# Kernel tuning notes

Hardware: AMD Instinct MI355X
Metric: run time of the kernel (lower is better)

## Reference

```python
import jax, jax.numpy as jnp
import numpy as np
from jax import lax

EPS = 1e-6


def _layernorm(x, g, b, eps=1e-5):
    m = x.mean(-1, keepdims=True)
    v = x.var(-1, keepdims=True)
    return (x - m) / jnp.sqrt(v + eps) * g + b


def _causal_conv(x, w, b, dilation):
    # x: [B,S,D], w: [K, D_in, D_out] -> causal (left) padded dilated conv + GELU, residual
    k = w.shape[0]
    pad = (k - 1) * dilation
    y = lax.conv_general_dilated(
        x, w, window_strides=(1,), padding=[(pad, 0)], rhs_dilation=(dilation,),
        dimension_numbers=('NWC', 'WIO', 'NWC'))
    return x + jax.nn.gelu(y + b)


def setup_inputs() -> dict:
    key = jax.random.key(0)
    B, S, D, DC, N_LTM, K_WM, KS = 4, 2048, 1024, 256, 768, 8, 5
    ks = jax.random.split(key, 24)
    sc = 0.02

    def n(k, shape, scale=sc):
        return jax.random.normal(k, shape, jnp.float32) * scale

    return {
        'x': jax.random.normal(ks[0], (B, S, D), jnp.float32),
        'cache': jax.random.normal(ks[1], (B, N_LTM, DC), jnp.float32),
        'wm': jax.random.normal(ks[2], (B, K_WM, DC + 1), jnp.float32),
        # LTM read projections
        'Wq_ltm': n(ks[3], (D, DC)), 'Wo_ltm': n(ks[4], (DC, D)), 'wg_ltm': n(ks[5], (D,)),
        # WM read projections
        'Wq_wm': n(ks[6], (D, DC)), 'Wo_wm': n(ks[7], (DC, D)), 'wg_wm': n(ks[8], (D,)),
        # causal dilated conv stack (2 layers, k=5, dilations 1 and 2)
        'conv1_w': n(ks[9], (KS, D, D)), 'conv1_b': jnp.zeros((D,), jnp.float32),
        'conv2_w': n(ks[10], (KS, D, D)), 'conv2_b': jnp.zeros((D,), jnp.float32),
        'ln_g': jnp.ones((D,), jnp.float32), 'ln_b': jnp.zeros((D,), jnp.float32),
        # WM write (learned slot keys for addressing)
        'Wqw_wm': n(ks[11], (D, DC)), 'Ww_wm': n(ks[12], (D, DC)),
        'wm_keys': n(ks[13], (K_WM, DC), 1.0), 'wgw_wm': n(ks[14], (D,)),
        # LTM write (content-based addressing against cache)
        'Wqw_ltm': n(ks[15], (D, DC)), 'Ww_ltm': n(ks[16], (D, DC)), 'wgw_ltm': n(ks[17], (D,)),
    }


def reference(x, cache, wm, Wq_ltm, Wo_ltm, wg_ltm, Wq_wm, Wo_wm, wg_wm,
              conv1_w, conv1_b, conv2_w, conv2_b, ln_g, ln_b,
              Wqw_wm, Ww_wm, wm_keys, wgw_wm, Wqw_ltm, Ww_ltm, wgw_ltm):
    DC = cache.shape[-1]
    inv_sqrt = 1.0 / jnp.sqrt(jnp.float32(DC))

    # ---- LTM READ: content-addressed soft read, gated residual blend ----
    q = x @ Wq_ltm                                                  # [B,S,DC]
    attn = jax.nn.softmax(jnp.einsum('bsd,bnd->bsn', q, cache) * inv_sqrt, -1)
    read = jnp.einsum('bsn,bnd->bsd', attn, cache)                  # [B,S,DC]
    gate = jax.nn.sigmoid(x @ wg_ltm)[..., None]                    # [B,S,1]
    x_ltm = x + gate * (read @ Wo_ltm)

    # ---- WM READ (read_decay=0.0 -> wm unchanged by read) ----
    content = wm[..., :DC]                                          # [B,Kw,DC]
    q2 = x_ltm @ Wq_wm
    attn2 = jax.nn.softmax(jnp.einsum('bsd,bkd->bsk', q2, content) * inv_sqrt, -1)
    read2 = jnp.einsum('bsk,bkd->bsd', attn2, content)
    gate2 = jax.nn.sigmoid(x_ltm @ wg_wm)[..., None]
    x_enh = x_ltm + gate2 * (read2 @ Wo_wm)

    # ---- COMPUTE: causal dilated conv stack + post-LayerNorm ----
    h = _causal_conv(x_enh, conv1_w, conv1_b, 1)
    h = _causal_conv(h, conv2_w, conv2_b, 2)
    out = _layernorm(h, ln_g, ln_b)                                 # [B,S,D]

    # ---- WM WRITE: gated soft-WTA addressing vs learned slot keys ----
    qw = out @ Wqw_wm                                               # [B,S,DC]
    aw = jax.nn.softmax(jnp.einsum('bsd,kd->bsk', qw, wm_keys) * inv_sqrt, -1)
    gw = jax.nn.sigmoid(out @ wgw_wm)[..., None]                    # [B,S,1]
    w = gw * aw                                                     # [B,S,Kw]
    tot = w.sum(1)                                                  # [B,Kw]
    c = out @ Ww_wm                                                 # [B,S,DC]
    avg = jnp.einsum('bsk,bsd->bkd', w, c) / (tot[..., None] + EPS)
    alpha = jnp.clip(tot, 0.0, 1.0)[..., None]
    new_content = (1.0 - alpha) * content + alpha * avg
    new_valid = jnp.clip(wm[..., DC] + tot, 0.0, 1.0)               # validity channel
    updated_wm = jnp.concatenate([new_content, new_valid[..., None]], -1)

    # ---- LTM WRITE: gated soft blended write, content-addressed vs cache ----
    ql = out @ Wqw_ltm
    al = jax.nn.softmax(jnp.einsum('bsd,bnd->bsn', ql, cache) * inv_sqrt, -1)
    gl = jax.nn.sigmoid(out @ wgw_ltm)[..., None]
    wl = gl * al                                                    # [B,S,N]
    totl = wl.sum(1)                                                # [B,N]
    cl = out @ Ww_ltm
    avgl = jnp.einsum('bsn,bsd->bnd', wl, cl) / (totl[..., None] + EPS)
    alphal = jnp.clip(totl, 0.0, 1.0)[..., None]
    updated_cache = (1.0 - alphal) * cache + alphal * avgl

    return (out, updated_cache, updated_wm)
```

## Files before the change

### kernel.cpp

```cpp
#include <hip/hip_runtime.h>
#include <stdint.h>

typedef unsigned short u16;
typedef unsigned int u32;
typedef __attribute__((ext_vector_type(8))) short s16x8;
typedef __attribute__((ext_vector_type(4))) float f32x4;

__device__ __forceinline__ float bf2f(u16 u) {
    return __builtin_bit_cast(float, (u32)u << 16);
}
__device__ __forceinline__ u16 f2bf(float f) {
    u32 u = __builtin_bit_cast(u32, f);
    u += 0x7FFFu + ((u >> 16) & 1u);
    return (u16)(u >> 16);
}
__device__ __forceinline__ void unpk4(uint2 r, float* o) {
    o[0] = bf2f((u16)(r.x & 0xffff)); o[1] = bf2f((u16)(r.x >> 16));
    o[2] = bf2f((u16)(r.y & 0xffff)); o[3] = bf2f((u16)(r.y >> 16));
}

__device__ __forceinline__ void gl16(const u16* g, u16* l) {
    __builtin_amdgcn_global_load_lds(
        (const __attribute__((address_space(1))) u32*)(const void*)g,
        (__attribute__((address_space(3))) u32*)(void*)l, 16, 0, 0);
}

#define BAR() { __builtin_amdgcn_sched_barrier(0); __builtin_amdgcn_s_barrier(); __builtin_amdgcn_sched_barrier(0); }

template<int DIL>
__global__ __launch_bounds__(512) void conv8_k(
    const u16* __restrict__ Apad, const u16* __restrict__ Bw,
    u16* __restrict__ Cb0, u16* __restrict__ Cb1)
{
    __shared__ u16 sA[2][16384];
    __shared__ u16 sB[2][16384];
    const int tid  = threadIdx.x;
    const int wid  = tid >> 6;
    const int lane = tid & 63;
    const int wr = (wid >> 2) * 128;
    const int wc = (wid & 3) * 64;
    const int lr = lane & 15;
    const int kq = lane >> 4;
    const int batch = blockIdx.x >> 3;
    const int m0b   = (blockIdx.x & 7) * 256;
    const int bn0   = blockIdx.y * 256;
    const int kbeg  = blockIdx.z * 2560;
    const u16* Ab = Apad + (long)batch * 2056 * 1024;

    const int row0 = tid >> 3;
    const int g0   = (tid & 7) ^ (row0 & 7);

    f32x4 acc[8][4] = {};
    s16x8 aF[4][2], bF[4][2];

    auto stageA = [&](int nb, int kt, int h) {
        const int ktabs = kbeg + kt * 64;
        const int tap = ktabs >> 10;
        const long rbase = (long)(8 + m0b + h * 128 + (tap - 4) * DIL) * 1024
                           + (ktabs & 1023) + g0 * 8;
        u16* dst = &sA[nb][h * 8192 + tid * 8];
        gl16(Ab + rbase + (long)row0 * 1024, dst);
        gl16(Ab + rbase + (long)(row0 + 64) * 1024, dst + 4096);
    };
    auto stageB = [&](int nb, int kt, int h) {
        const int ktabs = kbeg + kt * 64;
        const long rbase = (long)(bn0 + h * 128) * 5120 + ktabs + g0 * 8;
        u16* dst = &sB[nb][h * 8192 + tid * 8];
        gl16(Bw + rbase + (long)row0 * 5120, dst);
        gl16(Bw + rbase + (long)(row0 + 64) * 5120, dst + 4096);
    };
    auto readA = [&](int nb, int mq) {
        #pragma unroll
        for (int m = 0; m < 4; m++) {
            const int row = wr + (mq * 4 + m) * 16 + lr;
            #pragma unroll
            for (int ks = 0; ks < 2; ks++) {
                const int chunk = ks * 4 + kq;
                aF[m][ks] = *(const s16x8*)&sA[nb][row * 64 + ((chunk ^ (row & 7)) << 3)];
            }
        }
    };
    auto readB4 = [&](int nb, int nq) {
        #pragma unroll
        for (int n = 0; n < 2; n++) {
            const int row = wc + (nq * 2 + n) * 16 + lr;
            #pragma unroll
            for (int ks = 0; ks < 2; ks++) {
                const int chunk = ks * 4 + kq;
                bF[nq * 2 + n][ks] = *(const s16x8*)&sB[nb][row * 64 + ((chunk ^ (row & 7)) << 3)];
            }
        }
    };

#define MFQ(MQ, NQ) \
    { __builtin_amdgcn_s_setprio(1); \
      _Pragma("unroll") \
      for (int m = 0; m < 4; m++) { \
        _Pragma("unroll") \
        for (int n = 0; n < 2; n++) { \
          _Pragma("unroll") \
          for (int ks = 0; ks < 2; ks++) \
            acc[(MQ)*4+m][(NQ)*2+n] = __builtin_amdgcn_mfma_f32_16x16x32_bf16( \
                aF[m][ks], bF[(NQ)*2+n][ks], acc[(MQ)*4+m][(NQ)*2+n], 0, 0, 0); \
        } } \
      __builtin_amdgcn_s_setprio(0); }

    stageB(0, 0, 0); stageB(0, 0, 1); stageA(0, 0, 0); stageA(0, 0, 1);

    const int NT = 40;
    for (int t = 0; t < NT; ++t) {
        const int nb = t & 1;
        asm volatile("s_waitcnt vmcnt(4)" ::: "memory");
        BAR();
        readB4(nb, 0); readB4(nb, 1);
        if (t + 1 < NT) { stageB(nb ^ 1, t + 1, 0); stageB(nb ^ 1, t + 1, 1); }
        if (t + 1 < NT) { asm volatile("s_waitcnt vmcnt(4)" ::: "memory"); }
        else            { asm volatile("s_waitcnt vmcnt(0)" ::: "memory"); }
        BAR();
        readA(nb, 0);
        MFQ(0, 0); MFQ(0, 1);
        if (t + 1 < NT) { stageA(nb ^ 1, t + 1, 0); stageA(nb ^ 1, t + 1, 1); }
        readA(nb, 1);
        MFQ(1, 0); MFQ(1, 1);
    }
#undef MFQ

    u16* C = (blockIdx.z ? Cb1 : Cb0) + (long)batch * 2048 * 1024;
    #pragma unroll
    for (int m = 0; m < 8; m++) {
        #pragma unroll
        for (int n = 0; n < 4; n++) {
            const int cc = bn0 + wc + n * 16 + lr;
            #pragma unroll
            for (int j = 0; j < 4; j++) {
                const int r = m0b + wr + m * 16 + kq * 4 + j;
                C[(long)r * 1024 + cc] = f2bf(acc[m][n][j]);
            }
        }
    }
}

template<int AL, int BL, int EPI, int TN, int KS, int SWZ>
__global__ __launch_bounds__(256) void gemm_bf16(
    const u16* __restrict__ A, const u16* __restrict__ B,
    float* __restrict__ Cf, u16* __restrict__ Cb,
    const float* __restrict__ res, const float* __restrict__ gate,
    int M, int N, int K, int lda, int ldb,
    long aBS, long bBS, long cBS,
    u16* __restrict__ Pp, long pStride, int nby)
{
    constexpr int NFRAG = TN / 32;
    __shared__ u16 sA[128 * 32];
    __shared__ u16 sB[TN * 32];
    const int tid  = threadIdx.x;
    const int lane = tid & 63;
    const int wave = tid >> 6;
    const int wr = (wave >> 1) * 64;
    const int wc = (wave & 1) * (TN / 2);

    int bidx, bidy;
    if (SWZ) {
        const int nb  = gridDim.x;
        const int cpx = nb >> 3;
        const int bf  = blockIdx.x;
        const int sw  = (bf & 7) * cpx + (bf >> 3);
        bidx = sw / nby; bidy = sw - bidx * nby;
    } else {
        bidx = blockIdx.x; bidy = blockIdx.y;
    }
    const int m0 = bidx * 128;
    const int n0 = bidy * TN;
    const int zz = blockIdx.z;
    const long bz = (KS > 1) ? (zz / KS) : zz;
    const int ks  = (KS > 1) ? (zz % KS) : 0;
    const u16* Ab = A + bz * aBS;
    const u16* Bb = B + bz * bBS;

    f32x4 acc[4][NFRAG] = {};
    const int lr = lane & 15;
    const int lk = (lane >> 4) << 3;
    const int ar0 = tid >> 2;
    const int akg = (tid & 3) << 3;

    const int Kp = K / KS;
    const int kbeg = ks * Kp, kend = kbeg + Kp;

    for (int kk = kbeg; kk < kend; kk += 32) {
        __syncthreads();
        if (AL == 0) {
            gl16(Ab + (long)(m0 + ar0) * lda + kk + akg,      sA + tid * 8);
            gl16(Ab + (long)(m0 + ar0 + 64) * lda + kk + akg, sA + tid * 8 + 2048);
        } else {
            for (int t = tid; t < 512; t += 256) {
                int row = t & 127, kg = (t >> 7) << 3;
                u32 w0[4];
                #pragma unroll
                for (int j2 = 0; j2 < 4; j2++) {
                    u16 lo = Ab[(long)(kk + kg + 2*j2    ) * lda + m0 + row];
                    u16 hi = Ab[(long)(kk + kg + 2*j2 + 1) * lda + m0 + row];
                    w0[j2] = (u32)lo | ((u32)hi << 16);
                }
                uint4 v; v.x = w0[0]; v.y = w0[1]; v.z = w0[2]; v.w = w0[3];
                *reinterpret_cast<uint4*>(sA + row * 32 + kg) = v;
            }
        }
        if (BL == 1) {
            gl16(Bb + (long)(n0 + ar0) * ldb + kk + akg, sB + tid * 8);
            if (TN == 128)
                gl16(Bb + (long)(n0 + ar0 + 64) * ldb + kk + akg, sB + tid * 8 + 2048);
        } else {
            for (int t = tid; t < TN * 4; t += 256) {
                int col = t & (TN - 1), kg = (t / TN) << 3;
                u32 w0[4];
                #pragma unroll
                for (int j2 = 0; j2 < 4; j2++) {
                    u16 lo = Bb[(long)(kk + kg + 2*j2    ) * ldb + n0 + col];
                    u16 hi = Bb[(long)(kk + kg + 2*j2 + 1) * ldb + n0 + col];
                    w0[j2] = (u32)lo | ((u32)hi << 16);
                }
                uint4 v; v.x = w0[0]; v.y = w0[1]; v.z = w0[2]; v.w = w0[3];
                *reinterpret_cast<uint4*>(sB + col * 32 + kg) = v;
            }
        }
        __syncthreads();
        s16x8 aF[4], bF[NFRAG];
        #pragma unroll
        for (int m = 0; m < 4; m++)
            aF[m] = *reinterpret_cast<const s16x8*>(sA + (wr + m*16 + lr) * 32 + lk);
        #pragma unroll
        for (int n = 0; n < NFRAG; n++)
            bF[n] = *reinterpret_cast<const s16x8*>(sB + (wc + n*16 + lr) * 32 + lk);
        #pragma unroll
        for (int m = 0; m < 4; m++)
            #pragma unroll
            for (int n = 0; n < NFRAG; n++)
                acc[m][n] = __builtin_amdgcn_mfma_f32_16x16x32_bf16(aF[m], bF[n], acc[m][n], 0, 0, 0);
    }

    const int rj = (lane >> 4) << 2;
    if (KS > 1) {
        u16* Pb = Pp + (long)ks * pStride + bz * cBS;
        #pragma unroll
        for (int m = 0; m < 4; m++)
            #pragma unroll
            for (int n = 0; n < NFRAG; n++) {
                const int cc = n0 + wc + n*16 + lr;
                #pragma unroll
                for (int j = 0; j < 4; j++) {
                    const int r = m0 + wr + m*16 + rj + j;
                    Pb[(long)r * N + cc] = f2bf(acc[m][n][j]);
                }
            }
        return;
    }

    float* Cfb = Cf + bz * cBS;
    #pragma unroll
    for (int m = 0; m < 4; m++) {
        #pragma unroll
        for (int n = 0; n < NFRAG; n++) {
            const int cc = n0 + wc + n*16 + lr;
            #pragma unroll
            for (int j = 0; j < 4; j++) {
                const int r = m0 + wr + m*16 + rj + j;
                const long idx = (long)r * N + cc;
                const float v = acc[m][n][j];
                if (EPI == 0) {
                    Cb[bz * cBS + idx] = f2bf(v);
                } else if (EPI == 1) {
                    Cfb[idx] = v;
                } else {
                    float o = res[idx] + gate[r] * v;
                    Cfb[idx] = o;
                    if (EPI == 2) Cb[idx] = f2bf(o);
                }
            }
        }
    }
}

template<int KS, int BF>
__global__ __launch_bounds__(256) void ksum_k(
    const u16* __restrict__ Pp, long pStride,
    float* __restrict__ outf, u16* __restrict__ outb, int n4)
{
    int i = blockIdx.x * 256 + threadIdx.x;
    if (i >= n4) return;
    float s[4] = {0.f, 0.f, 0.f, 0.f};
    #pragma unroll
    for (int k = 0; k < KS; k++) {
        uint2 r = reinterpret_cast<const uint2*>(Pp + (long)k * pStride)[i];
        float v[4]; unpk4(r, v);
        s[0] += v[0]; s[1] += v[1]; s[2] += v[2]; s[3] += v[3];
    }
    if (BF) {
        u32 lo = (u32)f2bf(s[0]) | ((u32)f2bf(s[1]) << 16);
        u32 hi = (u32)f2bf(s[2]) | ((u32)f2bf(s[3]) << 16);
        reinterpret_cast<uint2*>(outb)[i] = make_uint2(lo, hi);
    } else {
        float4 o; o.x = s[0]; o.y = s[1]; o.z = s[2]; o.w = s[3];
        reinterpret_cast<float4*>(outf)[i] = o;
    }
}

__global__ __launch_bounds__(256) void prep_k(
    const float* __restrict__ x, const float* __restrict__ cache,
    const float* __restrict__ wm_keys, const float* __restrict__ wm,
    const float* __restrict__ Wo_wm, const float* __restrict__ Wq_wm,
    const float* __restrict__ Wq_ltm, const float* __restrict__ Wqw_wm,
    const float* __restrict__ Ww_wm, const float* __restrict__ Wqw_ltm,
    const float* __restrict__ Ww_ltm, const float* __restrict__ Wo_ltm,
    const float* __restrict__ conv1_w, const float* __restrict__ conv2_w,
    u16* __restrict__ xpad1, u16* __restrict__ xpad2,
    float* __restrict__ totl,
    u16* __restrict__ act0, u16* __restrict__ cache_b, u16* __restrict__ keys_b,
    u16* __restrict__ Wqb, u16* __restrict__ WbigT,
    u16* __restrict__ WoLt, u16* __restrict__ c1wt, u16* __restrict__ c2wt,
    u16* __restrict__ cache_t, float* __restrict__ CW, float* __restrict__ WC)
{
    __shared__ float tile[32][33];
    int b = blockIdx.x;
    int tid = threadIdx.x;

    if (b < 64) {
        int i = b * 256 + tid;
        int bt = i >> 12, j = i & 4095;
        long offp = (long)bt * (2056L * 1024 / 2) + j;
        reinterpret_cast<u32*>(xpad1)[offp] = 0u;
        reinterpret_cast<u32*>(xpad2)[offp] = 0u;
        if (i < 3072) totl[i] = 0.f;
        return;
    }
    b -= 64;
    if (b < 9218) {
        const float* in; u16* out; int i;
        if (b < 8192)      { in = x;       out = act0;    i = b * 256 + tid; }
        else if (b < 8960) { in = cache;   out = cache_b; i = (b - 8192) * 256 + tid; }
        else if (b < 8962) { in = wm_keys; out = keys_b;  i = (b - 8960) * 256 + tid; }
        else               { in = Wq_ltm;  out = Wqb;     i = (b - 8962) * 256 + tid; }
        float4 v = reinterpret_cast<const float4*>(in)[i];
        u32 lo = (u32)f2bf(v.x) | ((u32)f2bf(v.y) << 16);
        u32 hi = (u32)f2bf(v.z) | ((u32)f2bf(v.w) << 16);
        reinterpret_cast<uint2*>(out)[i] = make_uint2(lo, hi);
        return;
    }
    b -= 9218;
    if (b < 12288) {
        const float* in; u16* out; int R, C, l;
        if (b < 1024) {
            l = b & 255; R = 1024; C = 256;
            int m = b >> 8;
            if      (m == 0) { in = Wqw_wm;  out = WbigT; }
            else if (m == 1) { in = Ww_wm;   out = WbigT + 262144; }
            else if (m == 2) { in = Wqw_ltm; out = WbigT + 524288; }
            else             { in = Ww_ltm;  out = WbigT + 786432; }
        } else if (b < 1280) {
            l = b - 1024; in = Wo_ltm; out = WoLt; R = 256; C = 1024;
        } else if (b < 6400) {
            l = b - 1280; in = conv1_w; out = c1wt; R = 5120; C = 1024;
        } else if (b < 11520) {
            l = b - 6400; in = conv2_w; out = c2wt; R = 5120; C = 1024;
        } else {
            int lb = b - 11520;
            int z = lb / 192; l = lb % 192;
            in = cache + (long)z * 196608; out = cache_t + (long)z * 196608;
            R = 768; C = 256;
        }
        const int ct = C >> 5;
        const int c0 = (l % ct) * 32, r0 = (l / ct) * 32;
        int tx = tid & 31, ty = tid >> 5;
        #pragma unroll
        for (int i = 0; i < 32; i += 8)
            tile[ty + i][tx] = in[(long)(r0 + ty + i) * C + c0 + tx];
        __syncthreads();
        #pragma unroll
        for (int i = 0; i < 32; i += 8)
            out[(long)(c0 + ty + i) * R + r0 + tx] = f2bf(tile[tx][ty + i]);
        return;
    }
    b -= 12288;
    if (b < 32) {
        const float* wrow = wm + (long)(b >> 3) * 2056 + (b & 7) * 257;
        int c = tid;
        float a0 = 0.f, a1 = 0.f, a2 = 0.f, a3 = 0.f;
        for (int dd = 0; dd < 256; dd++) {
            float w = wrow[dd];
            const float* wo = Wo_wm + (long)dd * 1024;
            a0 += w * wo[c]; a1 += w * wo[c + 256];
            a2 += w * wo[c + 512]; a3 += w * wo[c + 768];
        }
        float* o = CW + (long)b * 1024;
        o[c] = a0; o[c + 256] = a1; o[c + 512] = a2; o[c + 768] = a3;
        return;
    }
    b -= 32;
    {
        const float* wrow = wm + (long)(b >> 3) * 2056 + (b & 7) * 257;
        int c = tid;
        float a0 = 0.f, a1 = 0.f, a2 = 0.f, a3 = 0.f;
        for (int j = 0; j < 256; j++) {
            float w = wrow[j];
            a0 += Wq_wm[(long)(c      ) * 256 + j] * w;
            a1 += Wq_wm[(long)(c + 256) * 256 + j] * w;
            a2 += Wq_wm[(long)(c + 512) * 256 + j] * w;
            a3 += Wq_wm[(long)(c + 768) * 256 + j] * w;
        }
        float* o = WC + (long)b * 1024;
        o[c] = a0; o[c + 256] = a1; o[c + 512] = a2; o[c + 768] = a3;
    }
}

__global__ __launch_bounds__(256) void gemv_sigmoid_k(
    const u16* __restrict__ X, const float* __restrict__ w,
    float* __restrict__ out)
{
    int row  = blockIdx.x * 4 + (threadIdx.x >> 6);
    int lane = threadIdx.x & 63;
    const u16* xr = X + (long)row * 1024;
    float s = 0.f;
    for (int i = lane * 4; i < 1024; i += 256) {
        uint2 r = *reinterpret_cast<const uint2*>(xr + i);
        float v[4]; unpk4(r, v);
        s += v[0]*w[i] + v[1]*w[i+1] + v[2]*w[i+2] + v[3]*w[i+3];
    }
    #pragma unroll
    for (int o = 32; o > 0; o >>= 1) s += __shfl_down(s, o);
    if (lane == 0) out[row] = 1.f / (1.f + __expf(-s));
}

__global__ __launch_bounds__(256) void softmax768_k(
    const u16* __restrict__ scores, u16* __restrict__ out,
    const float* __restrict__ gate)
{
    __shared__ float s4[4], s4b[4];
    int row = blockIdx.x;
    int t = threadIdx.x;
    const u16* sr = scores + (long)row * 768;
    float v[3];
    float m = -1e30f;
    #pragma unroll
    for (int i = 0; i < 3; i++) { v[i] = bf2f(sr[t + i*256]) * 0.0625f; m = fmaxf(m, v[i]); }
    float wm_ = m;
    #pragma unroll
    for (int o = 32; o > 0; o >>= 1) wm_ = fmaxf(wm_, __shfl_down(wm_, o));
    if ((t & 63) == 0) s4[t >> 6] = wm_;
    __syncthreads();
    float bm = fmaxf(fmaxf(s4[0], s4[1]), fmaxf(s4[2], s4[3]));
    float sum = 0.f;
    #pragma unroll
    for (int i = 0; i < 3; i++) { v[i] = __expf(v[i] - bm); sum += v[i]; }
    #pragma unroll
    for (int o = 32; o > 0; o >>= 1) sum += __shfl_down(sum, o);
    if ((t & 63) == 0) s4b[t >> 6] = sum;
    __syncthreads();
    float bs = s4b[0] + s4b[1] + s4b[2] + s4b[3];
    float g = gate ? gate[row] : 1.0f;
    float inv = g / bs;
    u16* orow = out + (long)row * 768;
    #pragma unroll
    for (int i = 0; i < 3; i++) orow[t + i*256] = f2bf(v[i] * inv);
}

__global__ __launch_bounds__(256) void wm_read_fused_k(
    const float* __restrict__ WC, const float* __restrict__ CW,
    const float* __restrict__ wg, const float* __restrict__ res,
    float* __restrict__ outf, u16* __restrict__ outb)
{
    __shared__ float sred[8][4];
    __shared__ float sg4[4];
    __shared__ float sa[8];
    __shared__ float gsh;
    int row = blockIdx.x;
    int b = row >> 11;
    int d = threadIdx.x, lane = d & 63, wave = d >> 6;
    long orow = (long)row * 1024;
    float rv0 = res[orow + d];
    float rv1 = res[orow + d + 256];
    float rv2 = res[orow + d + 512];
    float rv3 = res[orow + d + 768];
    float gp = rv0 * wg[d] + rv1 * wg[d + 256] + rv2 * wg[d + 512] + rv3 * wg[d + 768];
    #pragma unroll
    for (int o = 32; o > 0; o >>= 1) gp += __shfl_down(gp, o);
    if (lane == 0) sg4[wave] = gp;
    const float* wcb = WC + (long)b * 8192;
    #pragma unroll
    for (int k = 0; k < 8; k++) {
        const float* w = wcb + k * 1024;
        float v = rv0 * w[d] + rv1 * w[d + 256] + rv2 * w[d + 512] + rv3 * w[d + 768];
        #pragma unroll
        for (int o = 32; o > 0; o >>= 1) v += __shfl_down(v, o);
        if (lane == 0) sred[k][wave] = v;
    }
    __syncthreads();
    if (d < 8) sa[d] = (sred[d][0] + sred[d][1] + sred[d][2] + sred[d][3]) * 0.0625f;
    if (d == 0) gsh = 1.f / (1.f + __expf(-(sg4[0] + sg4[1] + sg4[2] + sg4[3])));
    __syncthreads();
    float m = sa[0];
    #pragma unroll
    for (int k = 1; k < 8; k++) m = fmaxf(m, sa[k]);
    float e[8], sum = 0.f;
    #pragma unroll
    for (int k = 0; k < 8; k++) { e[k] = __expf(sa[k] - m); sum += e[k]; }
    float inv = 1.f / sum;
    #pragma unroll
    for (int k = 0; k < 8; k++) e[k] *= inv;
    float g = gsh;
    const float* cwb = CW + (long)b * 8192;
    long prow = ((long)(row >> 11) * 2056 + 8 + (row & 2047)) * 1024;
    float rv[4] = { rv0, rv1, rv2, rv3 };
    #pragma unroll
    for (int j = 0; j < 4; j++) {
        int c = d + j * 256;
        float acc = 0.f;
        #pragma unroll
        for (int k = 0; k < 8; k++) acc += e[k] * cwb[k * 1024 + c];
        float o = rv[j] + g * acc;
        outf[orow + c] = o;
        outb[prow + c] = f2bf(o);
    }
}

template<int PAD>
__global__ __launch_bounds__(256) void gelu_reduce_k(
    const u16* __restrict__ p0, const u16* __restrict__ p1, const float4* __restrict__ res,
    const float* __restrict__ bias, float4* __restrict__ outf, u16* __restrict__ outb)
{
    int i4 = blockIdx.x * 256 + threadIdx.x;
    int r = i4 >> 8, c4 = (i4 & 255) << 2;
    float a[4], b[4];
    unpk4(reinterpret_cast<const uint2*>(p0)[i4], a);
    unpk4(reinterpret_cast<const uint2*>(p1)[i4], b);
    float4 rr = res[i4];
    float4 bi = *reinterpret_cast<const float4*>(bias + c4);
    float o[4];
    float y0 = a[0] + b[0] + bi.x, y1 = a[1] + b[1] + bi.y;
    float y2 = a[2] + b[2] + bi.z, y3 = a[3] + b[3] + bi.w;
    const float C0 = 0.79788456080286535588f, C1 = 0.044715f;
    o[0] = rr.x + 0.5f * y0 * (1.f + tanhf(C0 * (y0 + C1 * y0 * y0 * y0)));
    o[1] = rr.y + 0.5f * y1 * (1.f + tanhf(C0 * (y1 + C1 * y1 * y1 * y1)));
    o[2] = rr.z + 0.5f * y2 * (1.f + tanhf(C0 * (y2 + C1 * y2 * y2 * y2)));
    o[3] = rr.w + 0.5f * y3 * (1.f + tanhf(C0 * (y3 + C1 * y3 * y3 * y3)));
    float4 ov; ov.x = o[0]; ov.y = o[1]; ov.z = o[2]; ov.w = o[3];
    outf[i4] = ov;
    if (PAD) {
        long prow = ((long)(r >> 11) * 2056 + 8 + (r & 2047)) * 1024 + c4;
        u32 lo = (u32)f2bf(o[0]) | ((u32)f2bf(o[1]) << 16);
        u32 hi = (u32)f2bf(o[2]) | ((u32)f2bf(o[3]) << 16);
        *reinterpret_cast<uint2*>(outb + prow) = make_uint2(lo, hi);
    }
}

__global__ __launch_bounds__(256) void gelu_ln_k(
    const u16* __restrict__ p0, const u16* __restrict__ p1,
    const float4* __restrict__ res, const float* __restrict__ bias,
    const float* __restrict__ g, const float* __restrict__ b,
    float* __restrict__ outf, u16* __restrict__ outb)
{
    __shared__ float rs[4], rss[4];
    int row = blockIdx.x, t = threadIdx.x;
    long i4 = (long)row * 256 + t;
    float a[4], pb[4];
    unpk4(reinterpret_cast<const uint2*>(p0)[i4], a);
    unpk4(reinterpret_cast<const uint2*>(p1)[i4], pb);
    float4 rr = res[i4];
    float4 bi = reinterpret_cast<const float4*>(bias)[t];
    const float C0 = 0.79788456080286535588f, C1 = 0.044715f;
    float y0 = a[0] + pb[0] + bi.x, y1 = a[1] + pb[1] + bi.y;
    float y2 = a[2] + pb[2] + bi.z, y3 = a[3] + pb[3] + bi.w;
    float o0 = rr.x + 0.5f * y0 * (1.f + tanhf(C0 * (y0 + C1 * y0 * y0 * y0)));
    float o1 = rr.y + 0.5f * y1 * (1.f + tanhf(C0 * (y1 + C1 * y1 * y1 * y1)));
    float o2 = rr.z + 0.5f * y2 * (1.f + tanhf(C0 * (y2 + C1 * y2 * y2 * y2)));
    float o3 = rr.w + 0.5f * y3 * (1.f + tanhf(C0 * (y3 + C1 * y3 * y3 * y3)));
    float s  = o0 + o1 + o2 + o3;
    float ss = o0*o0 + o1*o1 + o2*o2 + o3*o3;
    #pragma unroll
    for (int o = 32; o > 0; o >>= 1) { s += __shfl_down(s, o); ss += __shfl_down(ss, o); }
    if ((t & 63) == 0) { rs[t >> 6] = s; rss[t >> 6] = ss; }
    __syncthreads();
    float S = rs[0]+rs[1]+rs[2]+rs[3];
    float SS = rss[0]+rss[1]+rss[2]+rss[3];
    float mean = S * (1.f/1024.f);
    float var  = SS * (1.f/1024.f) - mean*mean;
    float rstd = rsqrtf(var + 1e-5f);
    float4 gg = reinterpret_cast<const float4*>(g)[t];
    float4 bv = reinterpret_cast<const float4*>(b)[t];
    float4 y;
    y.x = (o0-mean)*rstd*gg.x + bv.x;
    y.y = (o1-mean)*rstd*gg.y + bv.y;
    y.z = (o2-mean)*rstd*gg.z + bv.z;
    y.w = (o3-mean)*rstd*gg.w + bv.w;
    reinterpret_cast<float4*>(outf)[i4] = y;
    u32 lo = (u32)f2bf(y.x) | ((u32)f2bf(y.y) << 16);
    u32 hi = (u32)f2bf(y.z) | ((u32)f2bf(y.w) << 16);
    reinterpret_cast<uint2*>(outb)[i4] = make_uint2(lo, hi);
}

__global__ __launch_bounds__(256) void attn8_wg_k(
    const u16* __restrict__ q, const float* __restrict__ xo,
    const float* __restrict__ w1, const float* __restrict__ w2,
    const u16* __restrict__ keys, float* __restrict__ wD,
    float* __restrict__ gateb2)
{
    __shared__ float sred[8][4];
    __shared__ float sa[8];
    __shared__ float sg1[4], sg2[4];
    __shared__ float g1sh;
    int row = blockIdx.x;
    int d = threadIdx.x, lane = d & 63, wave = d >> 6;
    float qv = bf2f(q[(long)row * 1024 + d]);
    float4 xr  = reinterpret_cast<const float4*>(xo + (long)row * 1024)[d];
    float4 w1v = reinterpret_cast<const float4*>(w1)[d];
    float4 w2v = reinterpret_cast<const float4*>(w2)[d];
    float s1 = xr.x*w1v.x + xr.y*w1v.y + xr.z*w1v.z + xr.w*w1v.w;
    float s2 = xr.x*w2v.x + xr.y*w2v.y + xr.z*w2v.z + xr.w*w2v.w;
    #pragma unroll
    for (int o = 32; o > 0; o >>= 1) { s1 += __shfl_down(s1, o); s2 += __shfl_down(s2, o); }
    if (lane == 0) { sg1[wave] = s1; sg2[wave] = s2; }
    #pragma unroll
    for (int k = 0; k < 8; k++) {
        float v = qv * bf2f(keys[k * 256 + d]);
        #pragma unroll
        for (int o = 32; o > 0; o >>= 1) v += __shfl_down(v, o);
        if (lane == 0) sred[k][wave] = v;
    }
    __syncthreads();
    if (d < 8) sa[d] = (sred[d][0] + sred[d][1] + sred[d][2] + sred[d][3]) * 0.0625f;
    if (d == 0) {
        g1sh = 1.f / (1.f + __expf(-(sg1[0] + sg1[1] + sg1[2] + sg1[3])));
        gateb2[row] = 1.f / (1.f + __expf(-(sg2[0] + sg2[1] + sg2[2] + sg2[3])));
    }
    __syncthreads();
    if (d < 8) {
        float m = sa[0];
        #pragma unroll
        for (int k = 1; k < 8; k++) m = fmaxf(m, sa[k]);
        float e = __expf(sa[d] - m), sum = 0.f;
        #pragma unroll
        for (int k = 0; k < 8; k++) sum += __expf(sa[k] - m);
        wD[(long)row * 8 + d] = g1sh * e / sum;
    }
}

__global__ __launch_bounds__(256) void wm_avg_partial_k(
    const float* __restrict__ wD, const u16* __restrict__ cw,
    float* __restrict__ part, float* __restrict__ part2)
{
    int blk = blockIdx.x;
    int b = blk >> 6, k = (blk >> 3) & 7, ch = blk & 7;
    int d = threadIdx.x;
    const float* wp = wD + ((long)b * 2048 + ch * 256) * 8 + k;
    const u16*   cp = cw + ((long)b * 2048 + ch * 256) * 1024 + 256 + d;
    float acc = 0.f, wsum = 0.f;
    for (int s = 0; s < 256; s++) {
        float wv = wp[s * 8];
        acc += wv * bf2f(cp[(long)s * 1024]);
        wsum += wv;
    }
    part[(long)blk * 256 + d] = acc;
    if (d == 0) part2[blk] = wsum;
}

__global__ __launch_bounds__(256) void wm_final_k(
    const float* __restrict__ part, const float* __restrict__ part2,
    const float* __restrict__ wm, float* __restrict__ out)
{
    int bk = blockIdx.x;
    int d = threadIdx.x;
    float acc = 0.f, t = 0.f;
    #pragma unroll
    for (int ch = 0; ch < 8; ch++) {
        acc += part[((long)bk * 8 + ch) * 256 + d];
        t   += part2[bk * 8 + ch];
    }
    float alpha = fminf(fmaxf(t, 0.f), 1.f);
    float avg = acc / (t + 1e-6f);
    long base = (long)(bk >> 3) * 2056 + (bk & 7) * 257;
    out[base + d] = (1.f - alpha) * wm[base + d] + alpha * avg;
    if (d == 0) out[base + 256] = fminf(fmaxf(wm[base + 256] + t, 0.f), 1.f);
}

__global__ void colsum_wl_k(const u16* __restrict__ wl, float* __restrict__ totl)
{
    int b = blockIdx.z;
    int n = blockIdx.x * 256 + threadIdx.x;
    int s0 = blockIdx.y * 256;
    const u16* p = wl + ((long)b * 2048 + s0) * 768 + n;
    float acc = 0.f;
    for (int s = 0; s < 256; s++) acc += bf2f(p[(long)s * 768]);
    atomicAdd(&totl[b * 768 + n], acc);
}

__global__ __launch_bounds__(256) void cache_blend_k(
    const float* __restrict__ cache, const u16* __restrict__ Pp, long pStride,
    const float* __restrict__ totl, float* __restrict__ out)
{
    int i4 = blockIdx.x * 256 + threadIdx.x;
    float s[4] = {0.f, 0.f, 0.f, 0.f};
    #pragma unroll
    for (int k = 0; k < 4; k++) {
        uint2 r = reinterpret_cast<const uint2*>(Pp + (long)k * pStride)[i4];
        float v[4]; unpk4(r, v);
        s[0] += v[0]; s[1] += v[1]; s[2] += v[2]; s[3] += v[3];
    }
    long i = (long)i4 * 4;
    int bn = (int)(i >> 8);
    float t = totl[bn];
    float a = fminf(fmaxf(t, 0.f), 1.f);
    float inv = a / (t + 1e-6f);
    float4 cv = reinterpret_cast<const float4*>(cache)[i4];
    float4 o;
    o.x = (1.f - a) * cv.x + s[0] * inv;
    o.y = (1.f - a) * cv.y + s[1] * inv;
    o.z = (1.f - a) * cv.z + s[2] * inv;
    o.w = (1.f - a) * cv.w + s[3] * inv;
    reinterpret_cast<float4*>(out)[i4] = o;
}

extern "C" void kernel_launch(void* const* d_in, const int* in_sizes, int n_in,
                              void* d_out, int out_size, void* d_ws, size_t ws_size,
                              hipStream_t stream)
{
    const int D = 1024, DC = 256, NL = 768;
    const long MS = 8192;
    const long SB = 2048;

    const float* x       = (const float*)d_in[0];
    const float* cache   = (const float*)d_in[1];
    const float* wm      = (const float*)d_in[2];
    const float* Wq_ltm  = (const float*)d_in[3];
    const float* Wo_ltm  = (const float*)d_in[4];
    const float* wg_ltm  = (const float*)d_in[5];
    const float* Wq_wm   = (const float*)d_in[6];
    const float* Wo_wm   = (const float*)d_in[7];
    const float* wg_wm   = (const float*)d_in[8];
    const float* conv1_w = (const float*)d_in[9];
    const float* conv1_b = (const float*)d_in[10];
    const float* conv2_w = (const float*)d_in[11];
    const float* conv2_b = (const float*)d_in[12];
    const float* ln_g    = (const float*)d_in[13];
    const float* ln_b    = (const float*)d_in[14];
    const float* Wqw_wm  = (const float*)d_in[15];
    const float* Ww_wm   = (const float*)d_in[16];
    const float* wm_keys = (const float*)d_in[17];
    const float* wgw_wm  = (const float*)d_in[18];
    const float* Wqw_ltm = (const float*)d_in[19];
    const float* Ww_ltm  = (const float*)d_in[20];
    const float* wgw_ltm = (const float*)d_in[21];

    float* out_f     = (float*)d_out;
    float* cache_out = out_f + 8388608;
    float* wm_out    = out_f + 8388608 + 786432;

    char* ws = (char*)d_ws;
    size_t off = 0;
    auto alloc = [&](size_t bytes) -> char* {
        char* p = ws + off;
        off = (off + bytes + 255) & ~(size_t)255;
        return p;
    };
    u16* Wqb     = (u16*)alloc((size_t)D*DC*2);
    u16* WoLt    = (u16*)alloc((size_t)D*DC*2);
    u16* WbigT   = (u16*)alloc((size_t)D*D*2);
    u16* c1wt    = (u16*)alloc((size_t)5*D*D*2);
    u16* c2wt    = (u16*)alloc((size_t)5*D*D*2);
    u16* cache_b = (u16*)alloc((size_t)4*NL*DC*2);
    u16* cache_t = (u16*)alloc((size_t)4*NL*DC*2);
    u16* keys_b  = (u16*)alloc((size_t)8*DC*2);
    u16* WqC     = (u16*)alloc((size_t)4*NL*D*2);
    u16* act0    = (u16*)alloc((size_t)MS*D*2);
    u16* act1    = (u16*)alloc((size_t)MS*D*2);
    u16* xpad1   = (u16*)alloc((size_t)4*2056*1024*2);
    u16* xpad2   = (u16*)alloc((size_t)4*2056*1024*2);
    u16* attnb   = (u16*)alloc((size_t)MS*NL*2);
    u16* readb   = (u16*)alloc((size_t)MS*DC*2);
    float* fact0 = (float*)alloc((size_t)MS*D*4);
    float* fact1 = (float*)alloc((size_t)MS*D*4);
    u16* Pu      = (u16*)alloc((size_t)16777216*2);
    float* CW    = (float*)alloc((size_t)4*8*D*4);
    float* WC    = (float*)alloc((size_t)4*8*D*4);
    float* gateb = (float*)alloc((size_t)MS*4);
    float* gateb2= (float*)alloc((size_t)MS*4);
    float* wD    = (float*)alloc((size_t)MS*8*4);
    float* totl  = (float*)alloc((size_t)4*NL*4);
    float* part  = (float*)alloc((size_t)256*256*4);
    float* part2 = (float*)alloc((size_t)256*4);
    u16*   qbig   = act0;

    prep_k<<<21634, 256, 0, stream>>>(
        x, cache, wm_keys, wm, Wo_wm, Wq_wm,
        Wq_ltm, Wqw_wm, Ww_wm, Wqw_ltm, Ww_ltm, Wo_ltm, conv1_w, conv2_w,
        xpad1, xpad2, totl, act0, cache_b, keys_b,
        Wqb, WbigT, WoLt, c1wt, c2wt, cache_t, CW, WC);

    gemm_bf16<0,1,0,128,1,0><<<dim3(6,8,4), 256, 0, stream>>>(
        cache_b, Wqb, nullptr, WqC, nullptr, nullptr,
        768,1024,256, 256,256, 196608L, 0L, 786432L, nullptr, 0, 0);
    gemv_sigmoid_k<<<2048, 256, 0, stream>>>(act0, wg_ltm, gateb);
    gemm_bf16<0,1,0,128,1,1><<<dim3(96,1,4), 256, 0, stream>>>(
        act0, WqC, nullptr, Pu, nullptr, nullptr,
        2048,768,1024, 1024,1024, SB*1024, 786432L, SB*768, nullptr, 0, 6);
    softmax768_k<<<8192, 256, 0, stream>>>(Pu, attnb, nullptr);
    gemm_bf16<0,1,0,64,2,1><<<dim3(64,1,8), 256, 0, stream>>>(
        attnb, cache_t, nullptr, nullptr, nullptr, nullptr,
        2048,256,768, 768,768, SB*768, (long)NL*DC, SB*256, Pu, 2097152L, 4);
    ksum_k<2,1><<<2048, 256, 0, stream>>>(Pu, 2097152L, nullptr, readb, 524288);
    gemm_bf16<0,1,5,128,1,1><<<dim3(512,1,1), 256, 0, stream>>>(
        readb, WoLt, fact0, nullptr, x, gateb,
        8192,1024,256, 256,256, 0,0,0, nullptr, 0, 8);

    wm_read_fused_k<<<8192, 256, 0, stream>>>(WC, CW, wg_wm, fact0, fact1, xpad1);

    conv8_k<1><<<dim3(32,4,2), 512, 0, stream>>>(xpad1, c1wt, Pu, Pu + 8388608);
    gelu_reduce_k<1><<<8192, 256, 0, stream>>>(
        Pu, Pu + 8388608, (const float4*)fact1, conv1_b, (float4*)fact0, xpad2);
    conv8_k<2><<<dim3(32,4,2), 512, 0, stream>>>(xpad2, c2wt, Pu, Pu + 8388608);
    gelu_ln_k<<<8192, 256, 0, stream>>>(
        Pu, Pu + 8388608, (const float4*)fact0, conv2_b, ln_g, ln_b, out_f, act1);

    gemm_bf16<0,1,0,128,1,1><<<dim3(512,1,1), 256, 0, stream>>>(
        act1, WbigT, nullptr, qbig, nullptr, nullptr,
        8192,1024,1024, 1024,1024, 0,0,0, nullptr, 0, 8);
    attn8_wg_k<<<8192, 256, 0, stream>>>(qbig, out_f, wgw_wm, wgw_ltm, keys_b, wD, gateb2);
    wm_avg_partial_k<<<256, 256, 0, stream>>>(wD, qbig, part, part2);
    wm_final_k<<<32, 256, 0, stream>>>(part, part2, wm, wm_out);

    gemm_bf16<0,1,0,128,1,1><<<dim3(96,1,4), 256, 0, stream>>>(
        qbig + 512, cache_b, nullptr, Pu, nullptr, nullptr,
        2048,768,256, 1024,256, SB*1024, (long)NL*DC, SB*768, nullptr, 0, 6);
    softmax768_k<<<8192, 256, 0, stream>>>(Pu, attnb, gateb2);
    colsum_wl_k<<<dim3(3, 8, 4), 256, 0, stream>>>(attnb, totl);
    gemm_bf16<1,0,1,64,4,0><<<dim3(6,4,16), 256, 0, stream>>>(
        attnb, qbig + 768, nullptr, nullptr, nullptr, nullptr,
        768,256,2048, 768,1024, SB*768, SB*1024, 196608L, Pu, 786432L, 0);
    cache_blend_k<<<768, 256, 0, stream>>>(cache, Pu, 786432L, totl, cache_out);

    (void)in_sizes; (void)n_in; (void)out_size; (void)ws_size;
}
```

Baseline: 504.9 us.

## Interleave conv GEMM staging with MFMAs and split-K the LTM score GEMM

The conv GEMM main loop now issues the next tile's B and A global-to-LDS loads in halves between MFMA groups, rather than in blocks before compute. A stageA2 helper changes the A row mapping to fit this schedule, and the wait counts are adjusted to match. Separately, the LTM read score GEMM gets a split-K of 2 writing bf16 partials, and the softmax kernel gains a template parameter that sums those partials on load. This aims to hide load latency and add parallelism to a small-grid GEMM, at the cost of extra partial-buffer traffic and some risk from the tighter vmcnt accounting.

```diff
diff --git a/kernel.cpp b/kernel.cpp
--- a/kernel.cpp
+++ b/kernel.cpp
@@ -53,14 +53,14 @@
     f32x4 acc[8][4] = {};
     s16x8 aF[4][2], bF[4][2];
 
-    auto stageA = [&](int nb, int kt, int h) {
+    auto stageA2 = [&](int nb, int kt, int c) {
         const int ktabs = kbeg + kt * 64;
         const int tap = ktabs >> 10;
-        const long rbase = (long)(8 + m0b + h * 128 + (tap - 4) * DIL) * 1024
+        const long rbase = (long)(8 + m0b + c * 64 + (tap - 4) * DIL) * 1024
                            + (ktabs & 1023) + g0 * 8;
-        u16* dst = &sA[nb][h * 8192 + tid * 8];
+        u16* dst = &sA[nb][(c * 64) * 64 + tid * 8];
         gl16(Ab + rbase + (long)row0 * 1024, dst);
-        gl16(Ab + rbase + (long)(row0 + 64) * 1024, dst + 4096);
+        gl16(Ab + rbase + (long)(row0 + 128) * 1024, dst + 8192);
     };
     auto stageB = [&](int nb, int kt, int h) {
         const int ktabs = kbeg + kt * 64;
@@ -105,23 +105,26 @@
         } } \
       __builtin_amdgcn_s_setprio(0); }
 
-    stageB(0, 0, 0); stageB(0, 0, 1); stageA(0, 0, 0); stageA(0, 0, 1);
+    stageB(0, 0, 0); stageB(0, 0, 1); stageA2(0, 0, 0); stageA2(0, 0, 1);
 
     const int NT = 40;
     for (int t = 0; t < NT; ++t) {
         const int nb = t & 1;
-        asm volatile("s_waitcnt vmcnt(4)" ::: "memory");
+        asm volatile("s_waitcnt vmcnt(2)" ::: "memory");
         BAR();
-        readB4(nb, 0); readB4(nb, 1);
-        if (t + 1 < NT) { stageB(nb ^ 1, t + 1, 0); stageB(nb ^ 1, t + 1, 1); }
+        readB4(nb, 0); readB4(nb, 1); readA(nb, 0);
+        if (t + 1 < NT) stageB(nb ^ 1, t + 1, 0);
+        MFQ(0, 0);
+        if (t + 1 < NT) stageB(nb ^ 1, t + 1, 1);
+        MFQ(0, 1);
         if (t + 1 < NT) { asm volatile("s_waitcnt vmcnt(4)" ::: "memory"); }
         else            { asm volatile("s_waitcnt vmcnt(0)" ::: "memory"); }
         BAR();
-        readA(nb, 0);
-        MFQ(0, 0); MFQ(0, 1);
-        if (t + 1 < NT) { stageA(nb ^ 1, t + 1, 0); stageA(nb ^ 1, t + 1, 1); }
         readA(nb, 1);
-        MFQ(1, 0); MFQ(1, 1);
+        if (t + 1 < NT) stageA2(nb ^ 1, t + 1, 0);
+        MFQ(1, 0);
+        if (t + 1 < NT) stageA2(nb ^ 1, t + 1, 1);
+        MFQ(1, 1);
     }
 #undef MFQ
 
@@ -428,8 +431,9 @@
     if (lane == 0) out[row] = 1.f / (1.f + __expf(-s));
 }
 
+template<int KS>
 __global__ __launch_bounds__(256) void softmax768_k(
-    const u16* __restrict__ scores, u16* __restrict__ out,
+    const u16* __restrict__ scores, long pStride, u16* __restrict__ out,
     const float* __restrict__ gate)
 {
     __shared__ float s4[4], s4b[4];
@@ -439,7 +443,12 @@
     float v[3];
     float m = -1e30f;
     #pragma unroll
-    for (int i = 0; i < 3; i++) { v[i] = bf2f(sr[t + i*256]) * 0.0625f; m = fmaxf(m, v[i]); }
+    for (int i = 0; i < 3; i++) {
+        float sv = bf2f(sr[t + i*256]);
+        #pragma unroll
+        for (int k = 1; k < KS; k++) sv += bf2f(sr[(long)k * pStride + t + i*256]);
+        v[i] = sv * 0.0625f; m = fmaxf(m, v[i]);
+    }
     float wm_ = m;
     #pragma unroll
     for (int o = 32; o > 0; o >>= 1) wm_ = fmaxf(wm_, __shfl_down(wm_, o));
@@ -796,10 +805,10 @@
         cache_b, Wqb, nullptr, WqC, nullptr, nullptr,
         768,1024,256, 256,256, 196608L, 0L, 786432L, nullptr, 0, 0);
     gemv_sigmoid_k<<<2048, 256, 0, stream>>>(act0, wg_ltm, gateb);
-    gemm_bf16<0,1,0,128,1,1><<<dim3(96,1,4), 256, 0, stream>>>(
-        act0, WqC, nullptr, Pu, nullptr, nullptr,
-        2048,768,1024, 1024,1024, SB*1024, 786432L, SB*768, nullptr, 0, 6);
-    softmax768_k<<<8192, 256, 0, stream>>>(Pu, attnb, nullptr);
+    gemm_bf16<0,1,0,128,2,1><<<dim3(96,1,8), 256, 0, stream>>>(
+        act0, WqC, nullptr, nullptr, nullptr, nullptr,
+        2048,768,1024, 1024,1024, SB*1024, 786432L, SB*768, Pu, 6291456L, 6);
+    softmax768_k<2><<<8192, 256, 0, stream>>>(Pu, 6291456L, attnb, nullptr);
     gemm_bf16<0,1,0,64,2,1><<<dim3(64,1,8), 256, 0, stream>>>(
         attnb, cache_t, nullptr, nullptr, nullptr, nullptr,
         2048,256,768, 768,768, SB*768, (long)NL*DC, SB*256, Pu, 2097152L, 4);
@@ -827,7 +836,7 @@
     gemm_bf16<0,1,0,128,1,1><<<dim3(96,1,4), 256, 0, stream>>>(
         qbig + 512, cache_b, nullptr, Pu, nullptr, nullptr,
         2048,768,256, 1024,256, SB*1024, (long)NL*DC, SB*768, nullptr, 0, 6);
-    softmax768_k<<<8192, 256, 0, stream>>>(Pu, attnb, gateb2);
+    softmax768_k<1><<<8192, 256, 0, stream>>>(Pu, 0L, attnb, gateb2);
     colsum_wl_k<<<dim3(3, 8, 4), 256, 0, stream>>>(attnb, totl);
     gemm_bf16<1,0,1,64,4,0><<<dim3(6,4,16), 256, 0, stream>>>(
         attnb, qbig + 768, nullptr, nullptr, nullptr, nullptr,
```

New measurement: 500.8 us. About the same (-0.8%).
